# Optimization experiments

Measured on AMD Instinct MI355X. Metric: run time of the kernel, lower is better.

The kernel has to match this reference:

```python
import jax, jax.numpy as jnp
import numpy as np

B, N, ME, D = 8, 1024, 1024, 1024

def setup_inputs() -> dict:
    key = jax.random.key(0)
    k1, k2, k3 = jax.random.split(key, 3)
    z = jax.random.normal(k1, (B, N, D), dtype=jnp.float32)
    e = jax.random.normal(k2, (B, ME, D), dtype=jnp.float32)
    M = jax.random.normal(k3, (D, D), dtype=jnp.float32)  # std=1 init as in torch code
    return {"z": z, "e": e, "M": M}

def reference(z, e, M):
    # a = z @ M @ e^T : [B, N, ME]
    a = jnp.einsum('bnd,de,bme->bnm', z, M, e)
    a = jax.nn.sigmoid(a)
    # softmax over dim=1 (the N / query axis), faithful to torch.softmax(a, dim=1)
    A = jax.nn.softmax(a, axis=1)
    e_out = jnp.einsum('bnm,bmd->bnd', A, e)
    return (e_out, A)
```

## Files before the change

kernel.cpp:

```cpp
#include <hip/hip_runtime.h>
#include <math.h>
#include <stdint.h>


typedef __bf16 bf16_8 __attribute__((ext_vector_type(8)));
typedef __bf16 bf16_4 __attribute__((ext_vector_type(4)));
typedef _Float16 f16_8 __attribute__((ext_vector_type(8)));
typedef _Float16 f16_4 __attribute__((ext_vector_type(4)));
typedef float  f32_4  __attribute__((ext_vector_type(4)));

__device__ __forceinline__ void gload_lds16(const void* g, void* l) {
    __builtin_amdgcn_global_load_lds(
        (const __attribute__((address_space(1))) void*)g,
        (__attribute__((address_space(3))) void*)l, 16, 0, 0);
}

__device__ __forceinline__ int swz8(int r) { return (r ^ (r >> 2)) & 7; }

template<typename T>
__device__ __forceinline__ void stage_16b(const T* __restrict__ g, int ldK,
                                          int k0, T* lds, int tid) {
#pragma unroll
    for (int t = 0; t < 4; ++t) {
        const int c = t * 256 + tid;
        const int row = c >> 3, slot = c & 7;
        gload_lds16(g + (long long)row * ldK + k0 + (slot ^ swz8(row)) * 8,
                    lds + (t * 256 + (tid >> 6) * 64) * 8);
    }
}

__device__ __forceinline__ void stage_f32_single(const float* __restrict__ g, int ldK,
                                                 int k0, _Float16* sH, int tid) {
#pragma unroll
    for (int p = 0; p < 8; ++p) {
        const int qi = p * 256 + tid;
        const int row = qi >> 4, kq4 = qi & 15;
        const float4 v = *(const float4*)(g + (long long)row * ldK + k0 + kq4 * 4);
        const int off = row * 64 + (((kq4 >> 1) ^ swz8(row)) * 8) + (kq4 & 1) * 4;
        f16_4 h;
        h[0] = (_Float16)v.x; h[1] = (_Float16)v.y;
        h[2] = (_Float16)v.z; h[3] = (_Float16)v.w;
        *(f16_4*)(sH + off) = h;
    }
}

__device__ __forceinline__ int frag_off(int r, int cK) {
    return r * 64 + ((cK ^ swz8(r)) * 8);
}

__global__ __launch_bounds__(256) void gemm1_kernel(
    const float* __restrict__ z, const _Float16* __restrict__ MT,
    _Float16* __restrict__ zM)
{
    const int D = 1024;
    __shared__ _Float16 sAh[8192], sBh[8192];
    const int tid = threadIdx.x, lane = tid & 63, w = tid >> 6;
    const int fr = lane & 15, q = lane >> 4;
    const int wr = (w >> 1) * 64, wc = (w & 1) * 64;
    const int rowb = blockIdx.x, colb = blockIdx.y;

    const float*    pA = z  + (long long)rowb * 128 * D;
    const _Float16* pB = MT + (long long)colb * 128 * D;

    f32_4 acc[4][4];
#pragma unroll
    for (int i = 0; i < 4; ++i)
#pragma unroll
        for (int j = 0; j < 4; ++j) acc[i][j] = (f32_4){0.f, 0.f, 0.f, 0.f};

    for (int k0 = 0; k0 < D; k0 += 64) {
        stage_16b(pB, D, k0, sBh, tid);
        stage_f32_single(pA, D, k0, sAh, tid);
        __syncthreads();
#pragma unroll
        for (int ch = 0; ch < 2; ++ch) {
            f16_8 ah[4], bh[4];
#pragma unroll
            for (int i = 0; i < 4; ++i) {
                ah[i] = *(const f16_8*)(sAh + frag_off(wr + 16 * i + fr, ch * 4 + q));
                bh[i] = *(const f16_8*)(sBh + frag_off(wc + 16 * i + fr, ch * 4 + q));
            }
#pragma unroll
            for (int i = 0; i < 4; ++i)
#pragma unroll
                for (int j = 0; j < 4; ++j)
                    acc[i][j] = __builtin_amdgcn_mfma_f32_16x16x32_f16(ah[i], bh[j], acc[i][j], 0, 0, 0);
        }
        __syncthreads();
    }

    const int row0 = rowb * 128 + wr;
    const int col0 = colb * 128 + wc;
#pragma unroll
    for (int i = 0; i < 4; ++i)
#pragma unroll
        for (int j = 0; j < 4; ++j) {
            const int col = col0 + 16 * j + fr;
#pragma unroll
            for (int reg = 0; reg < 4; ++reg) {
                const int row = row0 + 16 * i + q * 4 + reg;
                zM[(long long)row * D + col] = (_Float16)acc[i][j][reg];
            }
        }
}

__global__ __launch_bounds__(256) void gemm2_kernel(
    const _Float16* __restrict__ zM, const _Float16* __restrict__ e16,
    __bf16* __restrict__ P_bf, float* __restrict__ sums)
{
    const int D = 1024, N = 1024, ME = 1024;
    __shared__ _Float16 sAh[8192], sBh[8192];
    const int tid = threadIdx.x, lane = tid & 63, w = tid >> 6;
    const int fr = lane & 15, q = lane >> 4;
    const int wr = (w >> 1) * 64, wc = (w & 1) * 64;
    const int bz = blockIdx.x, rowb = blockIdx.y, colb = blockIdx.z;

    const _Float16* pA = zM  + ((long long)bz * N + rowb * 128) * D;
    const _Float16* pB = e16 + ((long long)bz * ME + colb * 128) * D;

    f32_4 acc[4][4];
#pragma unroll
    for (int i = 0; i < 4; ++i)
#pragma unroll
        for (int j = 0; j < 4; ++j) acc[i][j] = (f32_4){0.f, 0.f, 0.f, 0.f};

    for (int k0 = 0; k0 < D; k0 += 64) {
        stage_16b(pA, D, k0, sAh, tid);
        stage_16b(pB, D, k0, sBh, tid);
        __syncthreads();
#pragma unroll
        for (int ch = 0; ch < 2; ++ch) {
            f16_8 ah[4], bh[4];
#pragma unroll
            for (int i = 0; i < 4; ++i) {
                ah[i] = *(const f16_8*)(sAh + frag_off(wr + 16 * i + fr, ch * 4 + q));
                bh[i] = *(const f16_8*)(sBh + frag_off(wc + 16 * i + fr, ch * 4 + q));
            }
#pragma unroll
            for (int i = 0; i < 4; ++i)
#pragma unroll
                for (int j = 0; j < 4; ++j)
                    acc[i][j] = __builtin_amdgcn_mfma_f32_16x16x32_f16(ah[i], bh[j], acc[i][j], 0, 0, 0);
        }
        __syncthreads();
    }

    const int row0 = rowb * 128 + wr;
    const int col0 = colb * 128 + wc;
    float cs[4] = {0.f, 0.f, 0.f, 0.f};
#pragma unroll
    for (int i = 0; i < 4; ++i)
#pragma unroll
        for (int j = 0; j < 4; ++j) {
            const int col = col0 + 16 * j + fr;
#pragma unroll
            for (int reg = 0; reg < 4; ++reg) {
                const int row = row0 + 16 * i + q * 4 + reg;
                float v = acc[i][j][reg];
                const float s = 1.0f / (1.0f + __expf(-v));
                v = __expf(s);
                P_bf[(long long)bz * N * ME + (long long)row * ME + col] = (__bf16)v;
                cs[j] += v;
            }
        }
#pragma unroll
    for (int j = 0; j < 4; ++j) {
        float s = cs[j];
        s += __shfl_xor(s, 16, 64);
        s += __shfl_xor(s, 32, 64);
        if (lane < 16)
            atomicAdd(&sums[bz * ME + col0 + 16 * j + lane], s);
    }
}

__global__ __launch_bounds__(256) void escale_kernel(
    const float* __restrict__ e, const float* __restrict__ sums,
    __bf16* __restrict__ eTs)
{
    const int D = 1024, ME = 1024;
    __shared__ float t[64][33];
    const int b = blockIdx.x, m0 = blockIdx.y * 64, d0 = blockIdx.z * 32;
    const int tid = threadIdx.x;
    const float* eb = e + (long long)b * ME * D;
    const int tx = tid & 31, ty = tid >> 5;
#pragma unroll
    for (int rr = ty; rr < 64; rr += 8)
        t[rr][tx] = eb[(long long)(m0 + rr) * D + d0 + tx];
    const int wx = tid & 63, wy = tid >> 6;
    const float rs = 1.0f / sums[b * ME + m0 + wx];
    __syncthreads();
    __bf16* ob = eTs + (long long)b * D * ME;
#pragma unroll
    for (int dd = wy; dd < 32; dd += 4)
        ob[(long long)(d0 + dd) * ME + m0 + wx] = (__bf16)(t[wx][dd] * rs);
}

__global__ __launch_bounds__(256) void gemm3_kernel(
    const __bf16* __restrict__ P_bf, const __bf16* __restrict__ eTs,
    const float* __restrict__ sums,
    float* __restrict__ e_out, float* __restrict__ Aout)
{
    const int D = 1024, N = 1024, ME = 1024;
    const int tid = threadIdx.x;

    if (blockIdx.z >= 8) {
        const int b = blockIdx.x, yb = blockIdx.y, half = blockIdx.z - 8;
        const long long base = ((long long)b * N + yb * 128 + half * 64) * ME;
        const float4 sv = *(const float4*)(sums + b * ME + tid * 4);
        const float4 rs = make_float4(1.f / sv.x, 1.f / sv.y, 1.f / sv.z, 1.f / sv.w);
        for (int it = 0; it < 64; ++it) {
            const long long o = base + (long long)it * ME + tid * 4;
            bf16_4 p = *(const bf16_4*)(P_bf + o);
            *(float4*)(Aout + o) =
                make_float4((float)p[0] * rs.x, (float)p[1] * rs.y,
                            (float)p[2] * rs.z, (float)p[3] * rs.w);
        }
        return;
    }

    __shared__ __bf16 sA[8192], sB[8192];
    const int lane = tid & 63, w = tid >> 6;
    const int fr = lane & 15, q = lane >> 4;
    const int wr = (w >> 1) * 64, wc = (w & 1) * 64;
    const int bz = blockIdx.x, rowb = blockIdx.y, colb = blockIdx.z;

    const __bf16* pA = P_bf + ((long long)bz * N + rowb * 128) * ME;
    const __bf16* pB = eTs  + ((long long)bz * D + colb * 128) * ME;

    f32_4 acc[4][4];
#pragma unroll
    for (int i = 0; i < 4; ++i)
#pragma unroll
        for (int j = 0; j < 4; ++j) acc[i][j] = (f32_4){0.f, 0.f, 0.f, 0.f};

    for (int k0 = 0; k0 < ME; k0 += 64) {
        stage_16b(pA, ME, k0, sA, tid);
        stage_16b(pB, ME, k0, sB, tid);
        __syncthreads();
#pragma unroll
        for (int ch = 0; ch < 2; ++ch) {
            bf16_8 ah[4], bh[4];
#pragma unroll
            for (int i = 0; i < 4; ++i) {
                ah[i] = *(const bf16_8*)(sA + frag_off(wr + 16 * i + fr, ch * 4 + q));
                bh[i] = *(const bf16_8*)(sB + frag_off(wc + 16 * i + fr, ch * 4 + q));
            }
#pragma unroll
            for (int i = 0; i < 4; ++i)
#pragma unroll
                for (int j = 0; j < 4; ++j)
                    acc[i][j] = __builtin_amdgcn_mfma_f32_16x16x32_bf16(ah[i], bh[j], acc[i][j], 0, 0, 0);
        }
        __syncthreads();
    }

    const int row0 = rowb * 128 + wr;
    const int col0 = colb * 128 + wc;
#pragma unroll
    for (int i = 0; i < 4; ++i)
#pragma unroll
        for (int j = 0; j < 4; ++j) {
            const int col = col0 + 16 * j + fr;
#pragma unroll
            for (int reg = 0; reg < 4; ++reg) {
                const int row = row0 + 16 * i + q * 4 + reg;
                e_out[(long long)bz * N * D + (long long)row * D + col] = acc[i][j][reg];
            }
        }
}

__global__ __launch_bounds__(256) void prep_kernel(
    const float* __restrict__ M, _Float16* __restrict__ MT,
    const float* __restrict__ e, _Float16* __restrict__ e16,
    float* __restrict__ sums, int D)
{
    __shared__ float t32[32][33];
    const int bid = blockIdx.x, tid = threadIdx.x;
    if (bid < 1024) {
        const int r0 = (bid >> 5) * 32, c0 = (bid & 31) * 32;
        const int tx = tid & 31, ty = tid >> 5;
#pragma unroll
        for (int rr = ty; rr < 32; rr += 8)
            t32[rr][tx] = M[(long long)(r0 + rr) * D + c0 + tx];
        __syncthreads();
#pragma unroll
        for (int cc = ty; cc < 32; cc += 8) {
            const float v = t32[tx][cc];
            MT[(long long)(c0 + cc) * D + r0 + tx] = (_Float16)v;
        }
    } else if (bid < 1032) {
        const int i = ((bid - 1024) * 256 + tid) * 4;
        *(float4*)(sums + i) = make_float4(0.f, 0.f, 0.f, 0.f);
    } else {
        const long long base = (long long)(bid - 1032) * 4096;
#pragma unroll
        for (int p = 0; p < 4; ++p) {
            const long long i = base + (p * 256 + tid) * 4;
            const float4 v = *(const float4*)(e + i);
            f16_4 h;
            h[0] = (_Float16)v.x; h[1] = (_Float16)v.y;
            h[2] = (_Float16)v.z; h[3] = (_Float16)v.w;
            *(f16_4*)(e16 + i) = h;
        }
    }
}

#define TILE 128
#define KT 8
template<bool BT, int EPI>
__global__ __launch_bounds__(256) void gemm_kernel(
    const float* __restrict__ A, const float* __restrict__ B, float* __restrict__ C,
    long long sA, long long sB, long long sC, int Mrows, int Ncols, int K)
{
    __shared__ float As[KT][TILE + 4];
    __shared__ float Bs[KT][TILE + 4];
    const int bz = blockIdx.z;
    A += (long long)bz * sA; B += (long long)bz * sB; C += (long long)bz * sC;
    const int tid = threadIdx.x;
    const int row0 = blockIdx.y * TILE, col0 = blockIdx.x * TILE;
    const int ld_r = tid >> 1, ld_k4 = (tid & 1) * 4;
    const int bn_k = tid >> 5, bn_c4 = (tid & 31) * 4;
    const int tx = tid & 15, ty = tid >> 4;
    const int c0 = tx * 4, c1 = c0 + 64, r0 = ty * 4, r1 = r0 + 64;
    float acc[8][8];
#pragma unroll
    for (int i = 0; i < 8; i++)
#pragma unroll
        for (int j = 0; j < 8; j++) acc[i][j] = 0.f;
    for (int k0 = 0; k0 < K; k0 += KT) {
        float4 av = *(const float4*)(A + (long long)(row0 + ld_r) * K + k0 + ld_k4);
        float4 bv;
        if (BT) bv = *(const float4*)(B + (long long)(col0 + ld_r) * K + k0 + ld_k4);
        else    bv = *(const float4*)(B + (long long)(k0 + bn_k) * Ncols + col0 + bn_c4);
        __syncthreads();
        As[ld_k4 + 0][ld_r] = av.x; As[ld_k4 + 1][ld_r] = av.y;
        As[ld_k4 + 2][ld_r] = av.z; As[ld_k4 + 3][ld_r] = av.w;
        if (BT) {
            Bs[ld_k4 + 0][ld_r] = bv.x; Bs[ld_k4 + 1][ld_r] = bv.y;
            Bs[ld_k4 + 2][ld_r] = bv.z; Bs[ld_k4 + 3][ld_r] = bv.w;
        } else {
            *(float4*)&Bs[bn_k][bn_c4] = bv;
        }
        __syncthreads();
#pragma unroll
        for (int kk = 0; kk < KT; kk++) {
            float4 a0 = *(const float4*)&As[kk][r0];
            float4 a1 = *(const float4*)&As[kk][r1];
            float4 b0 = *(const float4*)&Bs[kk][c0];
            float4 b1 = *(const float4*)&Bs[kk][c1];
            float ar[8] = {a0.x, a0.y, a0.z, a0.w, a1.x, a1.y, a1.z, a1.w};
            float br[8] = {b0.x, b0.y, b0.z, b0.w, b1.x, b1.y, b1.z, b1.w};
#pragma unroll
            for (int i = 0; i < 8; i++)
#pragma unroll
                for (int j = 0; j < 8; j++) acc[i][j] += ar[i] * br[j];
        }
    }
#pragma unroll
    for (int i = 0; i < 8; i++) {
        const int rr = (i < 4) ? (r0 + i) : (r1 + i - 4);
        float* crow = C + (long long)(row0 + rr) * Ncols + col0;
        float v[8];
#pragma unroll
        for (int j = 0; j < 8; j++) v[j] = acc[i][j];
        if (EPI == 1) {
#pragma unroll
            for (int j = 0; j < 8; j++) {
                float s = 1.0f / (1.0f + __expf(-v[j]));
                v[j] = __expf(s);
            }
        }
        *(float4*)(crow + c0) = make_float4(v[0], v[1], v[2], v[3]);
        *(float4*)(crow + c1) = make_float4(v[4], v[5], v[6], v[7]);
    }
}

__global__ __launch_bounds__(256) void colsum_kernel(
    const float* __restrict__ P, float* __restrict__ sums, int Nn, int Mm, int chunk)
{
    const int g = blockIdx.x * 256 + threadIdx.x;
    const int b = g >> 10;
    const int m = g & 1023;
    const int n0 = blockIdx.y * chunk;
    const float* p = P + (long long)b * Nn * Mm + (long long)n0 * Mm + m;
    float s0 = 0.f, s1 = 0.f, s2 = 0.f, s3 = 0.f;
    for (int n = 0; n < chunk; n += 4) {
        s0 += p[(long long)(n + 0) * Mm];
        s1 += p[(long long)(n + 1) * Mm];
        s2 += p[(long long)(n + 2) * Mm];
        s3 += p[(long long)(n + 3) * Mm];
    }
    atomicAdd(&sums[g], (s0 + s1) + (s2 + s3));
}

__global__ __launch_bounds__(256) void scale_kernel(
    float* __restrict__ P, const float* __restrict__ sums)
{
    const long long base = (blockIdx.x * 256LL + threadIdx.x) * 4;
    const int b = (int)(base >> 20);
    const int col = (int)(base & 1023);
    float4 v = *(float4*)(P + base);
    const float4 s = *(const float4*)(sums + (b << 10) + col);
    v.x /= s.x; v.y /= s.y; v.z /= s.z; v.w /= s.w;
    *(float4*)(P + base) = v;
}

extern "C" void kernel_launch(void* const* d_in, const int* in_sizes, int n_in,
                              void* d_out, int out_size, void* d_ws, size_t ws_size,
                              hipStream_t stream)
{
    const int B = 8, N = 1024, ME = 1024, D = 1024;
    const float* z = (const float*)d_in[0];
    const float* e = (const float*)d_in[1];
    const float* M = (const float*)d_in[2];
    float* out   = (float*)d_out;
    float* e_out = out;
    float* Aout  = out + (long long)B * N * D;

    const size_t MB = 1024 * 1024;
    const size_t NEEDED = 52 * MB + (size_t)B * ME * sizeof(float);

    if (ws_size >= NEEDED) {
        char* W = (char*)d_ws;
        _Float16* MT   = (_Float16*)(W);
        _Float16* zM   = (_Float16*)(W + 4 * MB);
        _Float16* e16  = (_Float16*)(W + 20 * MB);
        __bf16*   P_bf = (__bf16*)(W + 36 * MB);
        float*    sums = (float*)(W + 52 * MB);
        __bf16*   eTs  = (__bf16*)zM;

        prep_kernel<<<dim3(3080), 256, 0, stream>>>(M, MT, e, e16, sums, D);

        gemm1_kernel<<<dim3(64, 8, 1), 256, 0, stream>>>(z, MT, zM);

        gemm2_kernel<<<dim3(8, 8, 8), 256, 0, stream>>>(zM, e16, P_bf, sums);

        escale_kernel<<<dim3(8, 16, 32), 256, 0, stream>>>(e, sums, eTs);

        gemm3_kernel<<<dim3(8, 8, 10), 256, 0, stream>>>(P_bf, eTs, sums, e_out, Aout);
    } else {
        float* zM   = (float*)d_ws;
        float* sums = (float*)((char*)d_ws + (size_t)B * N * D * 4);
        gemm_kernel<false, 0><<<dim3(ME / TILE, (B * N) / TILE, 1), 256, 0, stream>>>(
            z, M, zM, 0, 0, 0, B * N, D, D);
        gemm_kernel<true, 1><<<dim3(ME / TILE, N / TILE, B), 256, 0, stream>>>(
            zM, e, Aout, (long long)N * D, (long long)ME * D, (long long)N * ME, N, ME, D);
        hipMemsetAsync(sums, 0, (size_t)B * ME * sizeof(float), stream);
        colsum_kernel<<<dim3((B * ME) / 256, 8), 256, 0, stream>>>(Aout, sums, N, ME, N / 8);
        scale_kernel<<<dim3((B * N * ME / 4) / 256), 256, 0, stream>>>(Aout, sums);
        gemm_kernel<false, 0><<<dim3(D / TILE, N / TILE, B), 256, 0, stream>>>(
            Aout, e, e_out, (long long)N * ME, (long long)ME * D, (long long)N * D, N, D, ME);
    }
}
```

Measured before the change: 206.2 us.

## Pre-convert z to fp16, widen K-step to 128, move A normalization into escale

z is converted to fp16 in the prep kernel, so gemm1 stages both operands with direct global-to-LDS loads instead of converting fp32 in-loop. All three GEMMs now stage 128-wide K slices per barrier pair into doubled LDS buffers, which halves the number of synchronizations. The Aout normalization blocks move from gemm3 into escale_kernel, so gemm3 launches only GEMM tiles. The cost is 64KB of LDS per block, which may lower occupancy, plus an extra z conversion pass that reuses the P_bf buffer for z16.

```diff
diff --git a/kernel.cpp b/kernel.cpp
--- a/kernel.cpp
+++ b/kernel.cpp
@@ -29,38 +29,63 @@
     }
 }
 
-__device__ __forceinline__ void stage_f32_single(const float* __restrict__ g, int ldK,
-                                                 int k0, _Float16* sH, int tid) {
-#pragma unroll
-    for (int p = 0; p < 8; ++p) {
-        const int qi = p * 256 + tid;
-        const int row = qi >> 4, kq4 = qi & 15;
-        const float4 v = *(const float4*)(g + (long long)row * ldK + k0 + kq4 * 4);
-        const int off = row * 64 + (((kq4 >> 1) ^ swz8(row)) * 8) + (kq4 & 1) * 4;
-        f16_4 h;
-        h[0] = (_Float16)v.x; h[1] = (_Float16)v.y;
-        h[2] = (_Float16)v.z; h[3] = (_Float16)v.w;
-        *(f16_4*)(sH + off) = h;
-    }
-}
-
 __device__ __forceinline__ int frag_off(int r, int cK) {
     return r * 64 + ((cK ^ swz8(r)) * 8);
 }
 
+__device__ __forceinline__ void half_f16(const _Float16* sA_, const _Float16* sB_,
+                                         int wr, int wc, int fr, int q,
+                                         f32_4 acc[4][4])
+{
+#pragma unroll
+    for (int ch = 0; ch < 2; ++ch) {
+        f16_8 ah[4], bh[4];
+#pragma unroll
+        for (int i = 0; i < 4; ++i) {
+            ah[i] = *(const f16_8*)(sA_ + frag_off(wr + 16 * i + fr, ch * 4 + q));
+            bh[i] = *(const f16_8*)(sB_ + frag_off(wc + 16 * i + fr, ch * 4 + q));
+        }
+#pragma unroll
+        for (int i = 0; i < 4; ++i)
+#pragma unroll
+            for (int j = 0; j < 4; ++j)
+                acc[i][j] = __builtin_amdgcn_mfma_f32_16x16x32_f16(ah[i], bh[j], acc[i][j], 0, 0, 0);
+    }
+}
+
+__device__ __forceinline__ void half_bf16(const __bf16* sA_, const __bf16* sB_,
+                                          int wr, int wc, int fr, int q,
+                                          f32_4 acc[4][4])
+{
+#pragma unroll
+    for (int ch = 0; ch < 2; ++ch) {
+        bf16_8 ah[4], bh[4];
+#pragma unroll
+        for (int i = 0; i < 4; ++i) {
+            ah[i] = *(const bf16_8*)(sA_ + frag_off(wr + 16 * i + fr, ch * 4 + q));
+            bh[i] = *(const bf16_8*)(sB_ + frag_off(wc + 16 * i + fr, ch * 4 + q));
+        }
+#pragma unroll
+        for (int i = 0; i < 4; ++i)
+#pragma unroll
+            for (int j = 0; j < 4; ++j)
+                acc[i][j] = __builtin_amdgcn_mfma_f32_16x16x32_bf16(ah[i], bh[j], acc[i][j], 0, 0, 0);
+    }
+}
+
 __global__ __launch_bounds__(256) void gemm1_kernel(
-    const float* __restrict__ z, const _Float16* __restrict__ MT,
+    const _Float16* __restrict__ z16, const _Float16* __restrict__ MT,
     _Float16* __restrict__ zM)
 {
     const int D = 1024;
-    __shared__ _Float16 sAh[8192], sBh[8192];
+    __shared__ _Float16 sA0[8192], sA1[8192], sB0[8192], sB1[8192];
     const int tid = threadIdx.x, lane = tid & 63, w = tid >> 6;
     const int fr = lane & 15, q = lane >> 4;
     const int wr = (w >> 1) * 64, wc = (w & 1) * 64;
     const int rowb = blockIdx.x, colb = blockIdx.y;
 
-    const float*    pA = z  + (long long)rowb * 128 * D;
-    const _Float16* pB = MT + (long long)colb * 128 * D;
+    const _Float16* pA = z16 + (long long)rowb * 128 * D;
+    const _Float16* pB = MT  + (long long)colb * 128 * D;
 
     f32_4 acc[4][4];
 #pragma unroll
@@ -68,24 +93,14 @@
 #pragma unroll
         for (int j = 0; j < 4; ++j) acc[i][j] = (f32_4){0.f, 0.f, 0.f, 0.f};
 
-    for (int k0 = 0; k0 < D; k0 += 64) {
-        stage_16b(pB, D, k0, sBh, tid);
-        stage_f32_single(pA, D, k0, sAh, tid);
-        __syncthreads();
-#pragma unroll
-        for (int ch = 0; ch < 2; ++ch) {
-            f16_8 ah[4], bh[4];
-#pragma unroll
-            for (int i = 0; i < 4; ++i) {
-                ah[i] = *(const f16_8*)(sAh + frag_off(wr + 16 * i + fr, ch * 4 + q));
-                bh[i] = *(const f16_8*)(sBh + frag_off(wc + 16 * i + fr, ch * 4 + q));
-            }
-#pragma unroll
-            for (int i = 0; i < 4; ++i)
-#pragma unroll
-                for (int j = 0; j < 4; ++j)
-                    acc[i][j] = __builtin_amdgcn_mfma_f32_16x16x32_f16(ah[i], bh[j], acc[i][j], 0, 0, 0);
-        }
+    for (int k0 = 0; k0 < D; k0 += 128) {
+        stage_16b(pA, D, k0,      sA0, tid);
+        stage_16b(pA, D, k0 + 64, sA1, tid);
+        stage_16b(pB, D, k0,      sB0, tid);
+        stage_16b(pB, D, k0 + 64, sB1, tid);
+        __syncthreads();
+        half_f16(sA0, sB0, wr, wc, fr, q, acc);
+        half_f16(sA1, sB1, wr, wc, fr, q, acc);
         __syncthreads();
     }
 
@@ -109,7 +124,7 @@
     __bf16* __restrict__ P_bf, float* __restrict__ sums)
 {
     const int D = 1024, N = 1024, ME = 1024;
-    __shared__ _Float16 sAh[8192], sBh[8192];
+    __shared__ _Float16 sA0[8192], sA1[8192], sB0[8192], sB1[8192];
     const int tid = threadIdx.x, lane = tid & 63, w = tid >> 6;
     const int fr = lane & 15, q = lane >> 4;
     const int wr = (w >> 1) * 64, wc = (w & 1) * 64;
@@ -124,24 +139,14 @@
 #pragma unroll
         for (int j = 0; j < 4; ++j) acc[i][j] = (f32_4){0.f, 0.f, 0.f, 0.f};
 
-    for (int k0 = 0; k0 < D; k0 += 64) {
-        stage_16b(pA, D, k0, sAh, tid);
-        stage_16b(pB, D, k0, sBh, tid);
-        __syncthreads();
-#pragma unroll
-        for (int ch = 0; ch < 2; ++ch) {
-            f16_8 ah[4], bh[4];
-#pragma unroll
-            for (int i = 0; i < 4; ++i) {
-                ah[i] = *(const f16_8*)(sAh + frag_off(wr + 16 * i + fr, ch * 4 + q));
-                bh[i] = *(const f16_8*)(sBh + frag_off(wc + 16 * i + fr, ch * 4 + q));
-            }
-#pragma unroll
-            for (int i = 0; i < 4; ++i)
-#pragma unroll
-                for (int j = 0; j < 4; ++j)
-                    acc[i][j] = __builtin_amdgcn_mfma_f32_16x16x32_f16(ah[i], bh[j], acc[i][j], 0, 0, 0);
-        }
+    for (int k0 = 0; k0 < D; k0 += 128) {
+        stage_16b(pA, D, k0,      sA0, tid);
+        stage_16b(pA, D, k0 + 64, sA1, tid);
+        stage_16b(pB, D, k0,      sB0, tid);
+        stage_16b(pB, D, k0 + 64, sB1, tid);
+        __syncthreads();
+        half_f16(sA0, sB0, wr, wc, fr, q, acc);
+        half_f16(sA1, sB1, wr, wc, fr, q, acc);
         __syncthreads();
     }
 
@@ -175,36 +180,16 @@
 
 __global__ __launch_bounds__(256) void escale_kernel(
     const float* __restrict__ e, const float* __restrict__ sums,
-    __bf16* __restrict__ eTs)
-{
-    const int D = 1024, ME = 1024;
+    __bf16* __restrict__ eTs,
+    const __bf16* __restrict__ P_bf, float* __restrict__ Aout)
+{
+    const int D = 1024, ME = 1024, N = 1024;
     __shared__ float t[64][33];
-    const int b = blockIdx.x, m0 = blockIdx.y * 64, d0 = blockIdx.z * 32;
     const int tid = threadIdx.x;
-    const float* eb = e + (long long)b * ME * D;
-    const int tx = tid & 31, ty = tid >> 5;
-#pragma unroll
-    for (int rr = ty; rr < 64; rr += 8)
-        t[rr][tx] = eb[(long long)(m0 + rr) * D + d0 + tx];
-    const int wx = tid & 63, wy = tid >> 6;
-    const float rs = 1.0f / sums[b * ME + m0 + wx];
-    __syncthreads();
-    __bf16* ob = eTs + (long long)b * D * ME;
-#pragma unroll
-    for (int dd = wy; dd < 32; dd += 4)
-        ob[(long long)(d0 + dd) * ME + m0 + wx] = (__bf16)(t[wx][dd] * rs);
-}
-
-__global__ __launch_bounds__(256) void gemm3_kernel(
-    const __bf16* __restrict__ P_bf, const __bf16* __restrict__ eTs,
-    const float* __restrict__ sums,
-    float* __restrict__ e_out, float* __restrict__ Aout)
-{
-    const int D = 1024, N = 1024, ME = 1024;
-    const int tid = threadIdx.x;
-
-    if (blockIdx.z >= 8) {
-        const int b = blockIdx.x, yb = blockIdx.y, half = blockIdx.z - 8;
+
+    if (blockIdx.z >= 32) {
+        if (blockIdx.y >= 8) return;
+        const int b = blockIdx.x, yb = blockIdx.y, half = blockIdx.z - 32;
         const long long base = ((long long)b * N + yb * 128 + half * 64) * ME;
         const float4 sv = *(const float4*)(sums + b * ME + tid * 4);
         const float4 rs = make_float4(1.f / sv.x, 1.f / sv.y, 1.f / sv.z, 1.f / sv.w);
@@ -218,8 +203,28 @@
         return;
     }
 
-    __shared__ __bf16 sA[8192], sB[8192];
-    const int lane = tid & 63, w = tid >> 6;
+    const int b = blockIdx.x, m0 = blockIdx.y * 64, d0 = blockIdx.z * 32;
+    const float* eb = e + (long long)b * ME * D;
+    const int tx = tid & 31, ty = tid >> 5;
+#pragma unroll
+    for (int rr = ty; rr < 64; rr += 8)
+        t[rr][tx] = eb[(long long)(m0 + rr) * D + d0 + tx];
+    const int wx = tid & 63, wy = tid >> 6;
+    const float rs = 1.0f / sums[b * ME + m0 + wx];
+    __syncthreads();
+    __bf16* ob = eTs + (long long)b * D * ME;
+#pragma unroll
+    for (int dd = wy; dd < 32; dd += 4)
+        ob[(long long)(d0 + dd) * ME + m0 + wx] = (__bf16)(t[wx][dd] * rs);
+}
+
+__global__ __launch_bounds__(256) void gemm3_kernel(
+    const __bf16* __restrict__ P_bf, const __bf16* __restrict__ eTs,
+    float* __restrict__ e_out)
+{
+    const int D = 1024, N = 1024, ME = 1024;
+    __shared__ __bf16 sA0[8192], sA1[8192], sB0[8192], sB1[8192];
+    const int tid = threadIdx.x, lane = tid & 63, w = tid >> 6;
     const int fr = lane & 15, q = lane >> 4;
     const int wr = (w >> 1) * 64, wc = (w & 1) * 64;
     const int bz = blockIdx.x, rowb = blockIdx.y, colb = blockIdx.z;
@@ -233,24 +238,14 @@
 #pragma unroll
         for (int j = 0; j < 4; ++j) acc[i][j] = (f32_4){0.f, 0.f, 0.f, 0.f};
 
-    for (int k0 = 0; k0 < ME; k0 += 64) {
-        stage_16b(pA, ME, k0, sA, tid);
-        stage_16b(pB, ME, k0, sB, tid);
-        __syncthreads();
-#pragma unroll
-        for (int ch = 0; ch < 2; ++ch) {
-            bf16_8 ah[4], bh[4];
-#pragma unroll
-            for (int i = 0; i < 4; ++i) {
-                ah[i] = *(const bf16_8*)(sA + frag_off(wr + 16 * i + fr, ch * 4 + q));
-                bh[i] = *(const bf16_8*)(sB + frag_off(wc + 16 * i + fr, ch * 4 + q));
-            }
-#pragma unroll
-            for (int i = 0; i < 4; ++i)
-#pragma unroll
-                for (int j = 0; j < 4; ++j)
-                    acc[i][j] = __builtin_amdgcn_mfma_f32_16x16x32_bf16(ah[i], bh[j], acc[i][j], 0, 0, 0);
-        }
+    for (int k0 = 0; k0 < ME; k0 += 128) {
+        stage_16b(pA, ME, k0,      sA0, tid);
+        stage_16b(pA, ME, k0 + 64, sA1, tid);
+        stage_16b(pB, ME, k0,      sB0, tid);
+        stage_16b(pB, ME, k0 + 64, sB1, tid);
+        __syncthreads();
+        half_bf16(sA0, sB0, wr, wc, fr, q, acc);
+        half_bf16(sA1, sB1, wr, wc, fr, q, acc);
         __syncthreads();
     }
 
@@ -272,6 +267,7 @@
 __global__ __launch_bounds__(256) void prep_kernel(
     const float* __restrict__ M, _Float16* __restrict__ MT,
     const float* __restrict__ e, _Float16* __restrict__ e16,
+    const float* __restrict__ z, _Float16* __restrict__ z16,
     float* __restrict__ sums, int D)
 {
     __shared__ float t32[32][33];
@@ -291,7 +287,7 @@
     } else if (bid < 1032) {
         const int i = ((bid - 1024) * 256 + tid) * 4;
         *(float4*)(sums + i) = make_float4(0.f, 0.f, 0.f, 0.f);
-    } else {
+    } else if (bid < 3080) {
         const long long base = (long long)(bid - 1032) * 4096;
 #pragma unroll
         for (int p = 0; p < 4; ++p) {
@@ -301,6 +297,17 @@
             h[0] = (_Float16)v.x; h[1] = (_Float16)v.y;
             h[2] = (_Float16)v.z; h[3] = (_Float16)v.w;
             *(f16_4*)(e16 + i) = h;
+        }
+    } else {
+        const long long base = (long long)(bid - 3080) * 4096;
+#pragma unroll
+        for (int p = 0; p < 4; ++p) {
+            const long long i = base + (p * 256 + tid) * 4;
+            const float4 v = *(const float4*)(z + i);
+            f16_4 h;
+            h[0] = (_Float16)v.x; h[1] = (_Float16)v.y;
+            h[2] = (_Float16)v.z; h[3] = (_Float16)v.w;
+            *(f16_4*)(z16 + i) = h;
         }
     }
 }
@@ -427,17 +434,18 @@
         _Float16* e16  = (_Float16*)(W + 20 * MB);
         __bf16*   P_bf = (__bf16*)(W + 36 * MB);
         float*    sums = (float*)(W + 52 * MB);
+        _Float16* z16  = (_Float16*)P_bf;
         __bf16*   eTs  = (__bf16*)zM;
 
-        prep_kernel<<<dim3(3080), 256, 0, stream>>>(M, MT, e, e16, sums, D);
-
-        gemm1_kernel<<<dim3(64, 8, 1), 256, 0, stream>>>(z, MT, zM);
+        prep_kernel<<<dim3(5128), 256, 0, stream>>>(M, MT, e, e16, z, z16, sums, D);
+
+        gemm1_kernel<<<dim3(64, 8, 1), 256, 0, stream>>>(z16, MT, zM);
 
         gemm2_kernel<<<dim3(8, 8, 8), 256, 0, stream>>>(zM, e16, P_bf, sums);
 
-        escale_kernel<<<dim3(8, 16, 32), 256, 0, stream>>>(e, sums, eTs);
-
-        gemm3_kernel<<<dim3(8, 8, 10), 256, 0, stream>>>(P_bf, eTs, sums, e_out, Aout);
+        escale_kernel<<<dim3(8, 16, 34), 256, 0, stream>>>(e, sums, eTs, P_bf, Aout);
+
+        gemm3_kernel<<<dim3(8, 8, 8), 256, 0, stream>>>(P_bf, eTs, e_out);
     } else {
         float* zM   = (float*)d_ws;
         float* sums = (float*)((char*)d_ws + (size_t)B * N * D * 4);
```

Measured after the change: 197.3 us. 1.04x faster.
